# Performance work log

Hardware: AMD Instinct MI355X
Metric: run time of the kernel (lower is better)

Reference implementation:

```python
import jax, jax.numpy as jnp
import numpy as np

BN_EPS = 1e-5
NUM_SUBSET = 3


def conv1x1(x, w, b):
    # x: [N, C, T, V], w: [O, C], b: [O]  (1x1 Conv2d)
    return jnp.einsum('nctv,oc->notv', x, w) + b[:, None, None]


def setup_inputs() -> dict:
    key = jax.random.key(0)
    ks = jax.random.split(key, 8)
    N, C, T, V = 64, 64, 300, 25
    IC = 16  # inter_c = out_channels // coff_embedding
    O = 64
    inp = {
        'x': jax.random.normal(ks[0], (N, C, T, V), dtype=jnp.float32),
        'A': jax.random.uniform(ks[1], (NUM_SUBSET, V, V), dtype=jnp.float32),
        'graph_attn': jnp.ones((NUM_SUBSET, V, V), dtype=jnp.float32),
        'g_w': jax.random.normal(ks[2], (NUM_SUBSET, O, C), dtype=jnp.float32) * 0.05,
        'g_b': jnp.zeros((NUM_SUBSET, O), dtype=jnp.float32),
        'a_w': jax.random.normal(ks[3], (NUM_SUBSET, IC, C), dtype=jnp.float32) * 0.05,
        'a_b': jnp.zeros((NUM_SUBSET, IC), dtype=jnp.float32),
        'b_w': jax.random.normal(ks[4], (NUM_SUBSET, IC, C), dtype=jnp.float32) * 0.05,
        'b_b': jnp.zeros((NUM_SUBSET, IC), dtype=jnp.float32),
        'bn_gamma': jnp.ones((O,), dtype=jnp.float32),
        'bn_beta': jnp.zeros((O,), dtype=jnp.float32),
        'bn_mean': jnp.zeros((O,), dtype=jnp.float32),
        'bn_var': jnp.ones((O,), dtype=jnp.float32),
    }
    return inp


def reference(x, A, graph_attn, g_w, g_b, a_w, a_b, b_w, b_b,
              bn_gamma, bn_beta, bn_mean, bn_var):
    N, C, T, V = x.shape
    IC = a_w.shape[1]
    A_tot = A + graph_attn  # [3, V, V]
    x_flat = x.reshape(N, C * T, V)
    hidden = None
    for i in range(NUM_SUBSET):
        # a_conv -> permute(0,3,1,2) -> [N, V, IC*T]
        A1 = conv1x1(x, a_w[i], a_b[i]).transpose(0, 3, 1, 2).reshape(N, V, IC * T)
        # b_conv -> [N, IC*T, V]
        A2 = conv1x1(x, b_w[i], b_b[i]).reshape(N, IC * T, V)
        attn = jax.nn.softmax(jnp.matmul(A1, A2) / (IC * T), axis=-2)  # [N, V, V], softmax over rows
        attn = attn + A_tot[i]
        z = jnp.matmul(x_flat, attn).reshape(N, C, T, V)
        z = conv1x1(z, g_w[i], g_b[i])
        hidden = z if hidden is None else hidden + z
    # BatchNorm2d in eval mode over channel dim
    inv = jax.lax.rsqrt(bn_var + BN_EPS)
    hidden = (hidden - bn_mean[:, None, None]) * (inv * bn_gamma)[:, None, None] + bn_beta[:, None, None]
    # in_channels == out_channels -> identity residual
    hidden = hidden + x
    return jax.nn.relu(hidden)
```

## Files before the change

kernel.cpp:

```cpp
#include <hip/hip_runtime.h>
#include <hip/hip_bf16.h>


#define NB 64
#define CB 64
#define TB 300
#define VB 25
#define XTOT (NB * CB * TB * VB)

typedef unsigned int uint32;
typedef unsigned short ushort16;
typedef __attribute__((ext_vector_type(8))) short short8;
typedef __attribute__((ext_vector_type(4))) float f32x4;
typedef __attribute__((ext_vector_type(16))) float f32x16;

__device__ __forceinline__ ushort16 f2bf(float f) {
    __hip_bfloat16 h = __float2bfloat16(f);
    ushort16 u;
    __builtin_memcpy(&u, &h, sizeof(u));
    return u;
}
__device__ __forceinline__ float bf2f(ushort16 h) {
    return __uint_as_float(((uint32)h) << 16);
}
__device__ __forceinline__ uint32 packbf2(float a, float b) {
    return (uint32)f2bf(a) | ((uint32)f2bf(b) << 16);
}

__global__ __launch_bounds__(256) void k0_prep(
    const float* __restrict__ a_w, const float* __restrict__ b_w,
    const float* __restrict__ g_w,
    ushort16* __restrict__ wb2, uint32* __restrict__ gwb)
{
    int idx = blockIdx.x * 256 + threadIdx.x;
    if (idx < 6144) {
        int kb = idx / 768, rem = idx % 768;
        int r = rem >> 3, ci = rem & 7;
        int c = kb * 8 + ci;
        float v = (r < 48) ? a_w[r * 64 + c] : b_w[(r - 48) * 64 + c];
        wb2[idx] = f2bf(v);
    } else if (idx < 12288) {
        int j = idx - 6144;
        int o = j / 96, kp = j % 96;
        int k0 = 2 * kp, i = k0 >> 6, c = k0 & 63;
        float2 lh = *(const float2*)(g_w + (i * 64 + o) * 64 + c);
        gwb[j] = packbf2(lh.x, lh.y);
    }
}

__global__ __launch_bounds__(256) void k1_attn_logits_mfma(
    const float* __restrict__ x, const ushort16* __restrict__ wb2,
    const float* __restrict__ a_b, const float* __restrict__ b_b,
    float* __restrict__ Mp)
{
    __shared__ ushort16 pool[20352];
    ushort16* xT  = pool;
    ushort16* abT = pool + 126 * 64;

    const int tid   = threadIdx.x;
    const int n     = blockIdx.x / 25;
    const int chunk = blockIdx.x % 25;
    const float* xn = x + n * (CB * TB * VB);

    if (tid < 96) {
        float v = (tid < 48) ? a_b[tid] : b_b[tid - 48];
        ((float*)(abT + (31 + (tid >> 5) * 32) * 64))[tid & 31] = v;
    }

    const int w    = tid >> 6;
    const int lane = tid & 63;
    const int hi   = lane >> 5;
    const int v32  = lane & 31;

    const float* xb0 = xn + chunk * 12 * 25;

    const int tv     = w * 32 + v32;
    const bool avalid = tv < 100;
    const int tl = tv / 25;
    const int vv = tv - tl * 25;

    f32x16 accB;
    #pragma unroll
    for (int r = 0; r < 16; ++r) accB[r] = 0.f;

    for (int s = 0; s < 3; ++s) {
        __syncthreads();
        const float* xs0 = xb0 + s * 100;
        #pragma unroll
        for (int k = 0; k < 7; ++k) {
            int idx = tid + k * 256;
            if (idx < 1600) {
                int c = idx / 25, j = idx - c * 25;
                float4 v4 = *(const float4*)(xs0 + c * 7500 + j * 4);
                int sb   = ((c >> 3) + 5 * j) & 7;
                int base = (4 * j) * 64 + (c & 7);
                xT[base +   0 + (((sb + 0) & 7) << 3)] = f2bf(v4.x);
                xT[base +  64 + (((sb + 1) & 7) << 3)] = f2bf(v4.y);
                xT[base + 128 + (((sb + 2) & 7) << 3)] = f2bf(v4.z);
                xT[base + 192 + (((sb + 3) & 7) << 3)] = f2bf(v4.w);
            }
        }
        __syncthreads();
        #pragma unroll
        for (int rt = 0; rt < 3; ++rt) {
            f32x16 d;
            #pragma unroll
            for (int r = 0; r < 16; ++r) d[r] = 0.f;
            #pragma unroll
            for (int k16 = 0; k16 < 4; ++k16) {
                int kb = k16 * 2 + hi;
                short8 af = *(const short8*)(wb2 + (kb * 96 + rt * 32 + v32) * 8);
                short8 bf = *(const short8*)&xT[tv * 64 +
                                                (((kb + tv + (tv >> 2)) & 7) << 3)];
                d = __builtin_amdgcn_mfma_f32_32x32x16_bf16(af, bf, d, 0, 0, 0);
            }
            if (avalid) {
                #pragma unroll
                for (int a = 0; a < 4; ++a) {
                    int rowoff = 8 * a + 4 * hi;
                    int g   = rt * 2 + (rowoff >> 4);
                    int icb = rowoff & 15;
                    float4 bq = *(const float4*)(
                        (const float*)(abT + (31 + rt * 32) * 64) + rowoff);
                    int kbw = tl * 2 + (icb >> 3);
                    uint32* dst = (uint32*)&abT[(g * 32 + vv) * 64 +
                                                (((kbw + vv) & 7) << 3) + (icb & 7)];
                    dst[0] = packbf2(d[4 * a + 0] + bq.x, d[4 * a + 1] + bq.y);
                    dst[1] = packbf2(d[4 * a + 2] + bq.z, d[4 * a + 3] + bq.w);
                }
            }
        }
        __syncthreads();
        if (w < 3) {
            #pragma unroll
            for (int tl2 = 0; tl2 < 4; ++tl2) {
                int kb = tl2 * 2 + hi;
                short8 af = *(const short8*)&abT[(w * 32 + v32) * 64 +
                                                 (((kb + v32) & 7) << 3)];
                short8 bf = *(const short8*)&abT[((3 + w) * 32 + v32) * 64 +
                                                 (((kb + v32) & 7) << 3)];
                accB = __builtin_amdgcn_mfma_f32_32x32x16_bf16(af, bf, accB, 0, 0, 0);
            }
        }
    }

    if (w < 3 && v32 < 25) {
        const float inv = 1.0f / 4800.0f;
        float* dst = Mp + ((w * NB + n) * 25 + chunk) * 625;
        #pragma unroll
        for (int r = 0; r < 16; ++r) {
            int row = (r & 3) + 8 * (r >> 2) + 4 * hi;
            if (row < 25)
                dst[row * 25 + v32] = accB[r] * inv;
        }
    }
}

__global__ __launch_bounds__(128) void k2_softmax(
    const float* __restrict__ Mp, const float* __restrict__ A,
    const float* __restrict__ GA, uint32* __restrict__ atT)
{
    __shared__ float Ms[640];
    const int b   = blockIdx.x;
    const int tid = threadIdx.x;
    const int i = b >> 6, n = b & 63;
    const float* src = Mp + (size_t)b * 25 * 625;
    for (int idx = tid; idx < 625; idx += 128) {
        float ssum = 0.f;
        #pragma unroll 5
        for (int ch = 0; ch < 25; ++ch) ssum += src[ch * 625 + idx];
        Ms[idx] = ssum;
    }
    __syncthreads();
    if (tid < 25) {
        const int v2 = tid;
        float e[25], mx = -1e30f;
        #pragma unroll
        for (int v1 = 0; v1 < 25; ++v1) {
            e[v1] = Ms[v1 * 25 + v2];
            mx = fmaxf(mx, e[v1]);
        }
        float s = 0.f;
        #pragma unroll
        for (int v1 = 0; v1 < 25; ++v1) { e[v1] = __expf(e[v1] - mx); s += e[v1]; }
        float invs = 1.0f / s;
        const float* acol = A + i * 625 + v2;
        const float* gcol = GA + i * 625 + v2;
        float wv[25];
        #pragma unroll
        for (int v1 = 0; v1 < 25; ++v1)
            wv[v1] = e[v1] * invs + acol[v1 * 25] + gcol[v1 * 25];
        uint32* row = atT + ((i * 64 + n) * 32 + v2) * 16;
        #pragma unroll
        for (int p = 0; p < 12; ++p) row[p] = packbf2(wv[2 * p], wv[2 * p + 1]);
        row[12] = (uint32)f2bf(wv[24]);
        row[13] = 0u; row[14] = 0u; row[15] = 0u;
    }
}

__global__ __launch_bounds__(256) void k3_out(
    const float* __restrict__ x, const uint32* __restrict__ atT,
    const ushort16* __restrict__ gwb, const float* __restrict__ g_b,
    const float* __restrict__ bn_g, const float* __restrict__ bn_b,
    const float* __restrict__ bn_m, const float* __restrict__ bn_v,
    float* __restrict__ out)
{
    __shared__ uint32 xa[128 * 36];
    __shared__ float  bsc[64], bsh[64];

    const int tid = threadIdx.x;
    const int n  = blockIdx.x / 60;
    const int t0 = (blockIdx.x % 60) * 5;

    if (tid < 64) {
        float sc = bn_g[tid] * rsqrtf(bn_v[tid] + 1e-5f);
        bsc[tid] = sc;
        bsh[tid] = (g_b[tid] + g_b[64 + tid] + g_b[128 + tid] - bn_m[tid]) * sc
                   + bn_b[tid];
    }
    for (int idx = tid; idx < 108; idx += 256)
        xa[(125 + idx / 36) * 36 + idx % 36] = 0u;

    const int w    = tid >> 6;
    const int lane = tid & 63;
    const int l15  = lane & 15;
    const int q    = lane >> 4;

    short8 gf[6];
    #pragma unroll
    for (int s = 0; s < 6; ++s)
        gf[s] = *(const short8*)(gwb + ((w * 16 + l15) * 192 + s * 32 + q * 8));

    const int c    = w * 16 + l15;
    const int rowf = (n * 64 + c) * 7500 + t0 * 25;
    short8 axf[5];
    #pragma unroll
    for (int t = 0; t < 5; ++t) {
        int fi = rowf + t * 25 + q * 8;
        fi = fi < (XTOT - 8) ? fi : (XTOT - 8);
        const float* p = x + fi;
        union { short8 s; uint32 u[4]; } fr;
        fr.u[0] = packbf2(p[0], p[1]);
        fr.u[1] = packbf2(p[2], p[3]);
        fr.u[2] = packbf2(p[4], p[5]);
        fr.u[3] = packbf2(p[6], p[7]);
        axf[t] = fr.s;
    }

    f32x4 acc[8];
    #pragma unroll
    for (int ct = 0; ct < 8; ++ct) acc[ct] = (f32x4){0.f, 0.f, 0.f, 0.f};
    const f32x4 zf = (f32x4){0.f, 0.f, 0.f, 0.f};

    __syncthreads();

    for (int i = 0; i < 3; ++i) {
        if (i) __syncthreads();
        const ushort16* ap = (const ushort16*)atT + ((i * 64 + n) * 32) * 32;
        short8 bt0 = *(const short8*)(ap + l15 * 32 + q * 8);
        short8 bt1 = *(const short8*)(ap + (16 + l15) * 32 + q * 8);
        #pragma unroll
        for (int t = 0; t < 5; ++t) {
            #pragma unroll
            for (int vt = 0; vt < 2; ++vt) {
                f32x4 d = __builtin_amdgcn_mfma_f32_16x16x32_bf16(
                    axf[t], vt ? bt1 : bt0, zf, 0, 0, 0);
                int v2 = vt * 16 + l15;
                if (v2 < 25) {
                    int col = t * 25 + v2;
                    int c0  = w * 16 + q * 4;
                    xa[col * 36 + (c0 >> 1)]     = packbf2(d[0], d[1]);
                    xa[col * 36 + (c0 >> 1) + 1] = packbf2(d[2], d[3]);
                }
            }
        }
        __syncthreads();
        #pragma unroll
        for (int ct = 0; ct < 8; ++ct) {
            #pragma unroll
            for (int s = 0; s < 2; ++s) {
                short8 bfrag = *(const short8*)((const ushort16*)xa +
                                                (ct * 16 + l15) * 72 + s * 32 + q * 8);
                acc[ct] = __builtin_amdgcn_mfma_f32_16x16x32_bf16(
                    gf[i * 2 + s], bfrag, acc[ct], 0, 0, 0);
            }
        }
    }

    const int o0 = w * 16 + q * 4;
    #pragma unroll
    for (int ct = 0; ct < 8; ++ct) {
        int col = ct * 16 + l15;
        if (col < 125) {
            int off = (n * 64 + o0) * 7500 + t0 * 25 + col;
            float* ob = out + off;
            const float* xb = x + off;
            #pragma unroll
            for (int r = 0; r < 4; ++r) {
                float h = acc[ct][r] * bsc[o0 + r] + bsh[o0 + r] + xb[r * 7500];
                ob[r * 7500] = fmaxf(h, 0.f);
            }
        }
    }
}

extern "C" void kernel_launch(void* const* d_in, const int* in_sizes, int n_in,
                              void* d_out, int out_size, void* d_ws, size_t ws_size,
                              hipStream_t stream) {
    const float* x    = (const float*)d_in[0];
    const float* A    = (const float*)d_in[1];
    const float* GA   = (const float*)d_in[2];
    const float* g_w  = (const float*)d_in[3];
    const float* g_b  = (const float*)d_in[4];
    const float* a_w  = (const float*)d_in[5];
    const float* a_b  = (const float*)d_in[6];
    const float* b_w  = (const float*)d_in[7];
    const float* b_b  = (const float*)d_in[8];
    const float* bn_g = (const float*)d_in[9];
    const float* bn_b = (const float*)d_in[10];
    const float* bn_m = (const float*)d_in[11];
    const float* bn_v = (const float*)d_in[12];
    float* out = (float*)d_out;

    float*    Mp  = (float*)d_ws;
    uint32*   atT = (uint32*)((char*)d_ws + 12000000);
    ushort16* wb2 = (ushort16*)((char*)d_ws + 12000000);
    uint32*   gwb = (uint32*)((char*)d_ws + 12000000 + 393216);

    k0_prep<<<dim3(48), dim3(256), 0, stream>>>(a_w, b_w, g_w, wb2, gwb);
    k1_attn_logits_mfma<<<dim3(1600), dim3(256), 0, stream>>>(x, wb2, a_b, b_b, Mp);
    k2_softmax<<<dim3(192), dim3(128), 0, stream>>>(Mp, A, GA, atT);
    k3_out<<<dim3(3840), dim3(256), 0, stream>>>(x, atT, (const ushort16*)gwb,
                                                 g_b, bn_g, bn_b, bn_m, bn_v, out);
}
```

Before: 347.7 us.

## Prefetch next x slice during attention MFMA and vectorize partial-logit reduction

In the attention-logit kernel, the global loads of the next time slice are now issued before the A1·A2 MFMA steps, and their LDS stores come after them. This software-pipelines the memory latency behind compute and removes one barrier per iteration. The partial-logit buffer stride is padded from 625 to 640 floats so the softmax kernel can sum partials with float4 loads across 256 threads. The padding shifts the workspace offsets and adds register pressure from holding the prefetched values.

```diff
diff --git a/kernel.cpp b/kernel.cpp
--- a/kernel.cpp
+++ b/kernel.cpp
@@ -83,24 +83,45 @@
     #pragma unroll
     for (int r = 0; r < 16; ++r) accB[r] = 0.f;
 
+#define ST_LOADW(PV, K)                                                 \
+    {                                                                   \
+        int idx_ = tid + (K) * 256;                                     \
+        int c_ = idx_ / 25, j_ = idx_ - c_ * 25;                        \
+        float4 pv_ = (PV);                                              \
+        int sb_   = ((c_ >> 3) + 5 * j_) & 7;                           \
+        int base_ = (4 * j_) * 64 + (c_ & 7);                           \
+        xT[base_ +   0 + (((sb_ + 0) & 7) << 3)] = f2bf(pv_.x);         \
+        xT[base_ +  64 + (((sb_ + 1) & 7) << 3)] = f2bf(pv_.y);         \
+        xT[base_ + 128 + (((sb_ + 2) & 7) << 3)] = f2bf(pv_.z);         \
+        xT[base_ + 192 + (((sb_ + 3) & 7) << 3)] = f2bf(pv_.w);         \
+    }
+#define ST_LOAD(SRC, K)                                                 \
+    (*(const float4*)((SRC) + ((tid + (K) * 256) / 25) * 7500 +         \
+                      ((tid + (K) * 256) % 25) * 4))
+#define B_STEP(TL2)                                                     \
+    {                                                                   \
+        int kb_ = (TL2) * 2 + hi;                                       \
+        short8 af_ = *(const short8*)&abT[(w * 32 + v32) * 64 +         \
+                                          (((kb_ + v32) & 7) << 3)];    \
+        short8 bf_ = *(const short8*)&abT[((3 + w) * 32 + v32) * 64 +   \
+                                          (((kb_ + v32) & 7) << 3)];    \
+        accB = __builtin_amdgcn_mfma_f32_32x32x16_bf16(af_, bf_, accB,  \
+                                                       0, 0, 0);        \
+    }
+
+    {
+        const float* xs0 = xb0;
+        #pragma unroll
+        for (int k = 0; k < 7; ++k) {
+            if (k < 6 || tid < 64) {
+                float4 pv0 = ST_LOAD(xs0, k);
+                ST_LOADW(pv0, k)
+            }
+        }
+    }
+    __syncthreads();
+
     for (int s = 0; s < 3; ++s) {
-        __syncthreads();
-        const float* xs0 = xb0 + s * 100;
-        #pragma unroll
-        for (int k = 0; k < 7; ++k) {
-            int idx = tid + k * 256;
-            if (idx < 1600) {
-                int c = idx / 25, j = idx - c * 25;
-                float4 v4 = *(const float4*)(xs0 + c * 7500 + j * 4);
-                int sb   = ((c >> 3) + 5 * j) & 7;
-                int base = (4 * j) * 64 + (c & 7);
-                xT[base +   0 + (((sb + 0) & 7) << 3)] = f2bf(v4.x);
-                xT[base +  64 + (((sb + 1) & 7) << 3)] = f2bf(v4.y);
-                xT[base + 128 + (((sb + 2) & 7) << 3)] = f2bf(v4.z);
-                xT[base + 192 + (((sb + 3) & 7) << 3)] = f2bf(v4.w);
-            }
-        }
-        __syncthreads();
         #pragma unroll
         for (int rt = 0; rt < 3; ++rt) {
             f32x16 d;
@@ -131,22 +152,39 @@
             }
         }
         __syncthreads();
-        if (w < 3) {
-            #pragma unroll
-            for (int tl2 = 0; tl2 < 4; ++tl2) {
-                int kb = tl2 * 2 + hi;
-                short8 af = *(const short8*)&abT[(w * 32 + v32) * 64 +
-                                                 (((kb + v32) & 7) << 3)];
-                short8 bf = *(const short8*)&abT[((3 + w) * 32 + v32) * 64 +
-                                                 (((kb + v32) & 7) << 3)];
-                accB = __builtin_amdgcn_mfma_f32_32x32x16_bf16(af, bf, accB, 0, 0, 0);
-            }
+
+        if (s < 2) {
+            const float* xsN = xb0 + (s + 1) * 100;
+            {
+                float4 p0 = ST_LOAD(xsN, 0);
+                float4 p1 = ST_LOAD(xsN, 1);
+                float4 p2 = ST_LOAD(xsN, 2);
+                float4 p3 = ST_LOAD(xsN, 3);
+                if (w < 3) { B_STEP(0) B_STEP(1) }
+                ST_LOADW(p0, 0)
+                ST_LOADW(p1, 1)
+                ST_LOADW(p2, 2)
+                ST_LOADW(p3, 3)
+            }
+            {
+                float4 p4 = ST_LOAD(xsN, 4);
+                float4 p5 = ST_LOAD(xsN, 5);
+                float4 p6;
+                if (tid < 64) p6 = ST_LOAD(xsN, 6);
+                if (w < 3) { B_STEP(2) B_STEP(3) }
+                ST_LOADW(p4, 4)
+                ST_LOADW(p5, 5)
+                if (tid < 64) ST_LOADW(p6, 6)
+            }
+            __syncthreads();
+        } else {
+            if (w < 3) { B_STEP(0) B_STEP(1) B_STEP(2) B_STEP(3) }
         }
     }
 
     if (w < 3 && v32 < 25) {
         const float inv = 1.0f / 4800.0f;
-        float* dst = Mp + ((w * NB + n) * 25 + chunk) * 625;
+        float* dst = Mp + ((w * NB + n) * 25 + chunk) * 640;
         #pragma unroll
         for (int r = 0; r < 16; ++r) {
             int row = (r & 3) + 8 * (r >> 2) + 4 * hi;
@@ -154,22 +192,33 @@
                 dst[row * 25 + v32] = accB[r] * inv;
         }
     }
-}
-
-__global__ __launch_bounds__(128) void k2_softmax(
+#undef ST_LOADW
+#undef ST_LOAD
+#undef B_STEP
+}
+
+__global__ __launch_bounds__(256) void k2_softmax(
     const float* __restrict__ Mp, const float* __restrict__ A,
     const float* __restrict__ GA, uint32* __restrict__ atT)
 {
-    __shared__ float Ms[640];
+    __shared__ __align__(16) float Ms[640];
     const int b   = blockIdx.x;
     const int tid = threadIdx.x;
     const int i = b >> 6, n = b & 63;
-    const float* src = Mp + (size_t)b * 25 * 625;
-    for (int idx = tid; idx < 625; idx += 128) {
+    const float* src = Mp + (size_t)b * 25 * 640;
+    if (tid < 156) {
+        float4 a4 = make_float4(0.f, 0.f, 0.f, 0.f);
+        #pragma unroll 5
+        for (int ch = 0; ch < 25; ++ch) {
+            float4 v = *(const float4*)(src + ch * 640 + tid * 4);
+            a4.x += v.x; a4.y += v.y; a4.z += v.z; a4.w += v.w;
+        }
+        *(float4*)(Ms + tid * 4) = a4;
+    } else if (tid == 156) {
         float ssum = 0.f;
         #pragma unroll 5
-        for (int ch = 0; ch < 25; ++ch) ssum += src[ch * 625 + idx];
-        Ms[idx] = ssum;
+        for (int ch = 0; ch < 25; ++ch) ssum += src[ch * 640 + 624];
+        Ms[624] = ssum;
     }
     __syncthreads();
     if (tid < 25) {
@@ -323,13 +372,13 @@
     float* out = (float*)d_out;
 
     float*    Mp  = (float*)d_ws;
-    uint32*   atT = (uint32*)((char*)d_ws + 12000000);
-    ushort16* wb2 = (ushort16*)((char*)d_ws + 12000000);
-    uint32*   gwb = (uint32*)((char*)d_ws + 12000000 + 393216);
+    uint32*   atT = (uint32*)((char*)d_ws + 12288000);
+    ushort16* wb2 = (ushort16*)((char*)d_ws + 12288000);
+    uint32*   gwb = (uint32*)((char*)d_ws + 12288000 + 393216);
 
     k0_prep<<<dim3(48), dim3(256), 0, stream>>>(a_w, b_w, g_w, wb2, gwb);
     k1_attn_logits_mfma<<<dim3(1600), dim3(256), 0, stream>>>(x, wb2, a_b, b_b, Mp);
-    k2_softmax<<<dim3(192), dim3(128), 0, stream>>>(Mp, A, GA, atT);
+    k2_softmax<<<dim3(192), dim3(256), 0, stream>>>(Mp, A, GA, atT);
     k3_out<<<dim3(3840), dim3(256), 0, stream>>>(x, atT, (const ushort16*)gwb,
                                                  g_b, bn_g, bn_b, bn_m, bn_v, out);
 }
```

Measured after the change: 327.4 us. 5.8% less time.

## Load x fragments directly into registers in k1; pad partial logits for vector reduction

Applied to the files above, without the earlier changes.

The attention-logit kernel no longer stages a bf16-transposed tile of x in shared memory. Each lane now reads its MFMA B-operand elements straight from global memory (strided by channel) and packs them to bf16 in registers, which removes one LDS round trip and a barrier per step. The partial-logit buffer is padded to 640 floats per chunk so the softmax kernel can sum the partials with float4 loads across 256 threads. The direct loads are scalar and strided across channels, so they may coalesce worse than the old float4 staging loads.

```diff
diff --git a/kernel.cpp b/kernel.cpp
--- a/kernel.cpp
+++ b/kernel.cpp
@@ -53,9 +53,7 @@
     const float* __restrict__ a_b, const float* __restrict__ b_b,
     float* __restrict__ Mp)
 {
-    __shared__ ushort16 pool[20352];
-    ushort16* xT  = pool;
-    ushort16* abT = pool + 126 * 64;
+    __shared__ ushort16 abT[192 * 64];
 
     const int tid   = threadIdx.x;
     const int n     = blockIdx.x / 25;
@@ -72,35 +70,33 @@
     const int hi   = lane >> 5;
     const int v32  = lane & 31;
 
-    const float* xb0 = xn + chunk * 12 * 25;
-
-    const int tv     = w * 32 + v32;
+    const int tv      = w * 32 + v32;
     const bool avalid = tv < 100;
-    const int tl = tv / 25;
-    const int vv = tv - tl * 25;
+    const int tvc = avalid ? tv : 99;
+    const int tl  = tv / 25;
+    const int vv  = tv - tl * 25;
+
+    const float* xcol = xn + chunk * 300 + tvc;
 
     f32x16 accB;
     #pragma unroll
     for (int r = 0; r < 16; ++r) accB[r] = 0.f;
 
+    __syncthreads();
+
     for (int s = 0; s < 3; ++s) {
-        __syncthreads();
-        const float* xs0 = xb0 + s * 100;
-        #pragma unroll
-        for (int k = 0; k < 7; ++k) {
-            int idx = tid + k * 256;
-            if (idx < 1600) {
-                int c = idx / 25, j = idx - c * 25;
-                float4 v4 = *(const float4*)(xs0 + c * 7500 + j * 4);
-                int sb   = ((c >> 3) + 5 * j) & 7;
-                int base = (4 * j) * 64 + (c & 7);
-                xT[base +   0 + (((sb + 0) & 7) << 3)] = f2bf(v4.x);
-                xT[base +  64 + (((sb + 1) & 7) << 3)] = f2bf(v4.y);
-                xT[base + 128 + (((sb + 2) & 7) << 3)] = f2bf(v4.z);
-                xT[base + 192 + (((sb + 3) & 7) << 3)] = f2bf(v4.w);
-            }
-        }
-        __syncthreads();
+        const float* xs = xcol + s * 100;
+        short8 bfr[4];
+        #pragma unroll
+        for (int k16 = 0; k16 < 4; ++k16) {
+            const float* p = xs + (k16 * 2 + hi) * 8 * 7500;
+            union { short8 s8; uint32 u[4]; } fr;
+            fr.u[0] = packbf2(p[0],     p[7500]);
+            fr.u[1] = packbf2(p[15000], p[22500]);
+            fr.u[2] = packbf2(p[30000], p[37500]);
+            fr.u[3] = packbf2(p[45000], p[52500]);
+            bfr[k16] = fr.s8;
+        }
         #pragma unroll
         for (int rt = 0; rt < 3; ++rt) {
             f32x16 d;
@@ -110,9 +106,7 @@
             for (int k16 = 0; k16 < 4; ++k16) {
                 int kb = k16 * 2 + hi;
                 short8 af = *(const short8*)(wb2 + (kb * 96 + rt * 32 + v32) * 8);
-                short8 bf = *(const short8*)&xT[tv * 64 +
-                                                (((kb + tv + (tv >> 2)) & 7) << 3)];
-                d = __builtin_amdgcn_mfma_f32_32x32x16_bf16(af, bf, d, 0, 0, 0);
+                d = __builtin_amdgcn_mfma_f32_32x32x16_bf16(af, bfr[k16], d, 0, 0, 0);
             }
             if (avalid) {
                 #pragma unroll
@@ -142,11 +136,12 @@
                 accB = __builtin_amdgcn_mfma_f32_32x32x16_bf16(af, bf, accB, 0, 0, 0);
             }
         }
+        __syncthreads();
     }
 
     if (w < 3 && v32 < 25) {
         const float inv = 1.0f / 4800.0f;
-        float* dst = Mp + ((w * NB + n) * 25 + chunk) * 625;
+        float* dst = Mp + ((w * NB + n) * 25 + chunk) * 640;
         #pragma unroll
         for (int r = 0; r < 16; ++r) {
             int row = (r & 3) + 8 * (r >> 2) + 4 * hi;
@@ -156,20 +151,28 @@
     }
 }
 
-__global__ __launch_bounds__(128) void k2_softmax(
+__global__ __launch_bounds__(256) void k2_softmax(
     const float* __restrict__ Mp, const float* __restrict__ A,
     const float* __restrict__ GA, uint32* __restrict__ atT)
 {
-    __shared__ float Ms[640];
+    __shared__ __align__(16) float Ms[640];
     const int b   = blockIdx.x;
     const int tid = threadIdx.x;
     const int i = b >> 6, n = b & 63;
-    const float* src = Mp + (size_t)b * 25 * 625;
-    for (int idx = tid; idx < 625; idx += 128) {
+    const float* src = Mp + (size_t)b * 25 * 640;
+    if (tid < 156) {
+        float4 a4 = make_float4(0.f, 0.f, 0.f, 0.f);
+        #pragma unroll 5
+        for (int ch = 0; ch < 25; ++ch) {
+            float4 v = *(const float4*)(src + ch * 640 + tid * 4);
+            a4.x += v.x; a4.y += v.y; a4.z += v.z; a4.w += v.w;
+        }
+        *(float4*)(Ms + tid * 4) = a4;
+    } else if (tid == 156) {
         float ssum = 0.f;
         #pragma unroll 5
-        for (int ch = 0; ch < 25; ++ch) ssum += src[ch * 625 + idx];
-        Ms[idx] = ssum;
+        for (int ch = 0; ch < 25; ++ch) ssum += src[ch * 640 + 624];
+        Ms[624] = ssum;
     }
     __syncthreads();
     if (tid < 25) {
@@ -323,13 +326,13 @@
     float* out = (float*)d_out;
 
     float*    Mp  = (float*)d_ws;
-    uint32*   atT = (uint32*)((char*)d_ws + 12000000);
-    ushort16* wb2 = (ushort16*)((char*)d_ws + 12000000);
-    uint32*   gwb = (uint32*)((char*)d_ws + 12000000 + 393216);
+    uint32*   atT = (uint32*)((char*)d_ws + 12288000);
+    ushort16* wb2 = (ushort16*)((char*)d_ws + 12288000);
+    uint32*   gwb = (uint32*)((char*)d_ws + 12288000 + 393216);
 
     k0_prep<<<dim3(48), dim3(256), 0, stream>>>(a_w, b_w, g_w, wb2, gwb);
     k1_attn_logits_mfma<<<dim3(1600), dim3(256), 0, stream>>>(x, wb2, a_b, b_b, Mp);
-    k2_softmax<<<dim3(192), dim3(128), 0, stream>>>(Mp, A, GA, atT);
+    k2_softmax<<<dim3(192), dim3(256), 0, stream>>>(Mp, A, GA, atT);
     k3_out<<<dim3(3840), dim3(256), 0, stream>>>(x, atT, (const ushort16*)gwb,
                                                  g_b, bn_g, bn_b, bn_m, bn_v, out);
 }
```

New measurement: 324.4 us. -6.7%, faster.
